# Optimization experiments

Measured on AMD Instinct MI355X. Metric: run time of the kernel, lower is better.

## Reference

```python
import jax, jax.numpy as jnp
import numpy as np


def _maxpool2(t):
    # 2x2x2 max pool, stride 2. t: [B, C, D, H, W]
    B, C, D, H, W = t.shape
    return t.reshape(B, C, D // 2, 2, H // 2, 2, W // 2, 2).max(axis=(3, 5, 7))


def setup_inputs() -> dict:
    key = jax.random.key(0)
    ks = jax.random.split(key, 5)
    ch = 64
    B, D, H, W = 2, 32, 32, 32
    x = jax.random.normal(ks[0], (B, ch, D, H, W), dtype=jnp.float32)
    # 1x1x1 conv weights (out_ch, in_ch), Kaiming-ish scale
    w_theta = jax.random.normal(ks[1], (ch // 8, ch), dtype=jnp.float32) / np.sqrt(ch)
    w_phi = jax.random.normal(ks[2], (ch // 8, ch), dtype=jnp.float32) / np.sqrt(ch)
    w_g = jax.random.normal(ks[3], (ch // 2, ch), dtype=jnp.float32) / np.sqrt(ch)
    w_o = jax.random.normal(ks[4], (ch, ch // 2), dtype=jnp.float32) / np.sqrt(ch // 2)
    gamma = jnp.ones((), dtype=jnp.float32)  # original inits at 0; 1 gives nontrivial output
    return {"x": x, "w_theta": w_theta, "w_phi": w_phi, "w_g": w_g, "w_o": w_o, "gamma": gamma}


def reference(x, w_theta, w_phi, w_g, w_o, gamma):
    B, C, D, H, W = x.shape
    N = D * H * W
    M = N // 8
    xf = x.reshape(B, C, N)  # [B, C, N]
    # 1x1x1 convs = channel matmuls
    theta = jnp.einsum('oc,bcn->bon', w_theta, xf)                     # [B, C//8, N]
    phi = _maxpool2(jnp.einsum('oc,bcn->bon', w_phi, xf).reshape(B, C // 8, D, H, W)).reshape(B, C // 8, M)
    g = _maxpool2(jnp.einsum('oc,bcn->bon', w_g, xf).reshape(B, C // 2, D, H, W)).reshape(B, C // 2, M)
    # unscaled attention: softmax over keys (M)
    beta = jax.nn.softmax(jnp.einsum('bcn,bcm->bnm', theta, phi), axis=-1)  # [B, N, M]
    o = jnp.einsum('bcm,bnm->bcn', g, beta)                                 # [B, C//2, N]
    out = gamma * jnp.einsum('oc,bcn->bon', w_o, o).reshape(B, C, D, H, W) + x
    return out
```

## Files before the change

kernel.cpp:

```cpp
#include <hip/hip_runtime.h>
#include <cstdint>
#include <cstddef>

typedef __attribute__((ext_vector_type(4))) short short4v;
typedef __attribute__((ext_vector_type(4))) float float4v;

#define C_IN  64
#define NB    2
#define NPTS  32768
#define MPTS  4096
#define LOG2E 1.44269504088896340736f
#define KT    64
#define NTILE (MPTS / KT)
#define QT64  (NPTS / 64)

__device__ __forceinline__ unsigned short f2bf_rne(float f) {
  unsigned int u = __builtin_bit_cast(unsigned int, f);
  u += 0x7fffu + ((u >> 16) & 1u);
  return (unsigned short)(u >> 16);
}

__device__ __forceinline__ short4v pack_bf16_trunc(float a0, float a1, float a2, float a3) {
  unsigned int u0 = __builtin_amdgcn_perm(__builtin_bit_cast(unsigned int, a1),
                                          __builtin_bit_cast(unsigned int, a0), 0x07060302u);
  unsigned int u1 = __builtin_amdgcn_perm(__builtin_bit_cast(unsigned int, a3),
                                          __builtin_bit_cast(unsigned int, a2), 0x07060302u);
  union { unsigned int u[2]; short4v s; } r;
  r.u[0] = u0; r.u[1] = u1;
  return r.s;
}

__device__ __forceinline__ short4v pack_bf16_rne(float a0, float a1, float a2, float a3) {
  short4v s;
  s[0] = (short)f2bf_rne(a0); s[1] = (short)f2bf_rne(a1);
  s[2] = (short)f2bf_rne(a2); s[3] = (short)f2bf_rne(a3);
  return s;
}

__device__ __forceinline__ void gl_lds16(const unsigned short* g, unsigned short* l) {
  __builtin_amdgcn_global_load_lds(
      (const __attribute__((address_space(1))) void*)g,
      (__attribute__((address_space(3))) void*)l, 16, 0, 0);
}


__device__ void pool_body(int idx, const float* __restrict__ x,
                          const float* __restrict__ w_phi,
                          const float* __restrict__ w_g,
                          unsigned short* __restrict__ phi_f,
                          unsigned short* __restrict__ g_f) {
  int cg = idx >> 13;
  int bm = idx & 8191;
  int b = bm >> 12, m = bm & 4095;
  int md = m >> 8, mh = (m >> 4) & 15, mw = m & 15;
  const float* xb = x + (size_t)b * C_IN * NPTS
                  + ((md * 2) * 1024 + (mh * 2) * 32 + (mw * 2));
  const float* wbase = (cg == 0) ? w_phi : (w_g + (cg - 1) * 8 * C_IN);

  float acc[8][8];
#pragma unroll
  for (int o = 0; o < 8; ++o)
#pragma unroll
    for (int p = 0; p < 8; ++p) acc[o][p] = 0.f;

#pragma unroll 4
  for (int cc = 0; cc < C_IN; ++cc) {
    const float* xp = xb + (size_t)cc * NPTS;
    float2 p01 = *(const float2*)(xp + 0);
    float2 p23 = *(const float2*)(xp + 32);
    float2 p45 = *(const float2*)(xp + 1024);
    float2 p67 = *(const float2*)(xp + 1056);
#pragma unroll
    for (int o = 0; o < 8; ++o) {
      float wv = wbase[o * C_IN + cc];
      acc[o][0] = fmaf(wv, p01.x, acc[o][0]);
      acc[o][1] = fmaf(wv, p01.y, acc[o][1]);
      acc[o][2] = fmaf(wv, p23.x, acc[o][2]);
      acc[o][3] = fmaf(wv, p23.y, acc[o][3]);
      acc[o][4] = fmaf(wv, p45.x, acc[o][4]);
      acc[o][5] = fmaf(wv, p45.y, acc[o][5]);
      acc[o][6] = fmaf(wv, p67.x, acc[o][6]);
      acc[o][7] = fmaf(wv, p67.y, acc[o][7]);
    }
  }
  float mx[8];
#pragma unroll
  for (int o = 0; o < 8; ++o) {
    mx[o] = fmaxf(fmaxf(fmaxf(acc[o][0], acc[o][1]), fmaxf(acc[o][2], acc[o][3])),
                  fmaxf(fmaxf(acc[o][4], acc[o][5]), fmaxf(acc[o][6], acc[o][7])));
  }
  int kt16 = m >> 4, kr = m & 15;
  if (cg == 0) {
    size_t fb = ((size_t)b * 256 + kt16) * 256;
#pragma unroll
    for (int g2 = 0; g2 < 2; ++g2) {
      unsigned int u0 = (unsigned int)f2bf_rne(mx[g2 * 4 + 0] * LOG2E)
                      | ((unsigned int)f2bf_rne(mx[g2 * 4 + 1] * LOG2E) << 16);
      unsigned int u1 = (unsigned int)f2bf_rne(mx[g2 * 4 + 2] * LOG2E)
                      | ((unsigned int)f2bf_rne(mx[g2 * 4 + 3] * LOG2E) << 16);
      *(uint2*)&phi_f[fb + (g2 * 16 + kr) * 4] = make_uint2(u0, u1);
      *(uint2*)&phi_f[fb + ((g2 + 2) * 16 + kr) * 4] = make_uint2(0u, 0u);
    }
  } else {
    int gc0 = (cg - 1) * 8;
#pragma unroll
    for (int o = 0; o < 8; ++o) {
      int c = gc0 + o;
      int half = c >> 4, c15 = c & 15;
      size_t base = (((size_t)b * 256 + kt16) * 2 + half) * 256;
      g_f[base + ((kr >> 2) * 16 + c15) * 4 + (kr & 3)] = f2bf_rne(mx[o]);
    }
  }
}

__device__ void theta_body(int idx, const float* __restrict__ x,
                           const float* __restrict__ w_theta,
                           unsigned short* __restrict__ theta_pad) {
  int b = idx >> 15, n = idx & 32767;
  const float* xb = x + (size_t)b * C_IN * NPTS + n;
  float t[8];
#pragma unroll
  for (int o = 0; o < 8; ++o) t[o] = 0.f;
#pragma unroll 4
  for (int cc = 0; cc < C_IN; ++cc) {
    float xv = xb[(size_t)cc * NPTS];
#pragma unroll
    for (int o = 0; o < 8; ++o) t[o] = fmaf(w_theta[o * C_IN + cc], xv, t[o]);
  }
  unsigned int w0 = (unsigned int)f2bf_rne(t[0]) | ((unsigned int)f2bf_rne(t[1]) << 16);
  unsigned int w1 = (unsigned int)f2bf_rne(t[2]) | ((unsigned int)f2bf_rne(t[3]) << 16);
  unsigned int w2 = (unsigned int)f2bf_rne(t[4]) | ((unsigned int)f2bf_rne(t[5]) << 16);
  unsigned int w3 = (unsigned int)f2bf_rne(t[6]) | ((unsigned int)f2bf_rne(t[7]) << 16);
  uint4* dst = (uint4*)(theta_pad + ((size_t)idx << 4));
  dst[0] = make_uint4(w0, w1, w2, w3);
  dst[1] = make_uint4(0u, 0u, 0u, 0u);
}

__global__ __launch_bounds__(256) void prep_fused(
    const float* __restrict__ x, const float* __restrict__ w_theta,
    const float* __restrict__ w_phi, const float* __restrict__ w_g,
    unsigned short* __restrict__ theta_pad,
    unsigned short* __restrict__ phi_f,
    unsigned short* __restrict__ g_f) {
  int gb = blockIdx.x;
  if (gb < 160) {
    pool_body(gb * 256 + threadIdx.x, x, w_phi, w_g, phi_f, g_f);
  } else {
    theta_body((gb - 160) * 256 + threadIdx.x, x, w_theta, theta_pad);
  }
}

template <int KS>
__global__ __launch_bounds__(256, 4) void attn_split64(
    const unsigned short* __restrict__ theta_pad,
    const unsigned short* __restrict__ phi_f,
    const unsigned short* __restrict__ g_f,
    float4v* __restrict__ opart,
    float* __restrict__ lbuf) {
  __shared__ unsigned short s_phi[2][KT * 16];
  __shared__ unsigned short s_g[2][(KT / 16) * 512];

  int tid = threadIdx.x;
  int wid = tid >> 6, lane = tid & 63;
  int l4 = lane >> 4, col = lane & 15;
  int b = blockIdx.y / KS;
  int ks = blockIdx.y % KS;
  int qb = blockIdx.x * 256 + wid * 64;
  int qt64 = blockIdx.x * 4 + wid;
  int t0 = ks * (NTILE / KS);
  int t1 = t0 + NTILE / KS;

  const unsigned short* tb = theta_pad + ((size_t)(b * NPTS + qb) << 4) + l4 * 4;
  short4v bt0 = *(const short4v*)(tb + ((0 * 16 + col) << 4));
  short4v bt1 = *(const short4v*)(tb + ((1 * 16 + col) << 4));
  short4v bt2 = *(const short4v*)(tb + ((2 * 16 + col) << 4));
  short4v bt3 = *(const short4v*)(tb + ((3 * 16 + col) << 4));

  const unsigned short* phib = phi_f + (size_t)b * 65536;
  const unsigned short* gb   = g_f + (size_t)b * 131072;

  float4v acc[2][4];
#pragma unroll
  for (int h = 0; h < 2; ++h)
#pragma unroll
    for (int j = 0; j < 4; ++j) acc[h][j] = (float4v){0.f, 0.f, 0.f, 0.f};
  float lsum0 = 0.f, lsum1 = 0.f, lsum2 = 0.f, lsum3 = 0.f;

  gl_lds16(gb + (size_t)t0 * 2048 + wid * 512 + lane * 8, &s_g[0][wid * 512]);
  if (wid < 2)
    gl_lds16(phib + (size_t)t0 * 1024 + wid * 512 + lane * 8, &s_phi[0][wid * 512]);
  __syncthreads();

#pragma unroll 1
  for (int t = t0; t < t1; ++t) {
    int cur = t & 1;
    if (t + 1 < t1) {
      gl_lds16(gb + (size_t)(t + 1) * 2048 + wid * 512 + lane * 8,
               &s_g[cur ^ 1][wid * 512]);
      if (wid < 2)
        gl_lds16(phib + (size_t)(t + 1) * 1024 + wid * 512 + lane * 8,
                 &s_phi[cur ^ 1][wid * 512]);
    }

#pragma unroll
    for (int st = 0; st < 4; ++st) {
      short4v pf = *(const short4v*)&s_phi[cur][st * 256 + lane * 4];
      short4v g0 = *(const short4v*)&s_g[cur][st * 512 + lane * 4];
      short4v g1 = *(const short4v*)&s_g[cur][st * 512 + 256 + lane * 4];

      float4v zero4 = {0.f, 0.f, 0.f, 0.f};
      float4v s0 = __builtin_amdgcn_mfma_f32_16x16x16bf16_1k(pf, bt0, zero4, 0, 0, 0);
      float4v s1 = __builtin_amdgcn_mfma_f32_16x16x16bf16_1k(pf, bt1, zero4, 0, 0, 0);
      float4v s2 = __builtin_amdgcn_mfma_f32_16x16x16bf16_1k(pf, bt2, zero4, 0, 0, 0);
      float4v s3 = __builtin_amdgcn_mfma_f32_16x16x16bf16_1k(pf, bt3, zero4, 0, 0, 0);

      float p00 = __builtin_amdgcn_exp2f(s0[0]);
      float p01 = __builtin_amdgcn_exp2f(s0[1]);
      float p02 = __builtin_amdgcn_exp2f(s0[2]);
      float p03 = __builtin_amdgcn_exp2f(s0[3]);
      float p10 = __builtin_amdgcn_exp2f(s1[0]);
      float p11 = __builtin_amdgcn_exp2f(s1[1]);
      float p12 = __builtin_amdgcn_exp2f(s1[2]);
      float p13 = __builtin_amdgcn_exp2f(s1[3]);
      float p20 = __builtin_amdgcn_exp2f(s2[0]);
      float p21 = __builtin_amdgcn_exp2f(s2[1]);
      float p22 = __builtin_amdgcn_exp2f(s2[2]);
      float p23 = __builtin_amdgcn_exp2f(s2[3]);
      float p30 = __builtin_amdgcn_exp2f(s3[0]);
      float p31 = __builtin_amdgcn_exp2f(s3[1]);
      float p32 = __builtin_amdgcn_exp2f(s3[2]);
      float p33 = __builtin_amdgcn_exp2f(s3[3]);
      lsum0 += (p00 + p01) + (p02 + p03);
      lsum1 += (p10 + p11) + (p12 + p13);
      lsum2 += (p20 + p21) + (p22 + p23);
      lsum3 += (p30 + p31) + (p32 + p33);
      short4v pb0 = pack_bf16_trunc(p00, p01, p02, p03);
      short4v pb1 = pack_bf16_trunc(p10, p11, p12, p13);
      short4v pb2 = pack_bf16_trunc(p20, p21, p22, p23);
      short4v pb3 = pack_bf16_trunc(p30, p31, p32, p33);

      acc[0][0] = __builtin_amdgcn_mfma_f32_16x16x16bf16_1k(g0, pb0, acc[0][0], 0, 0, 0);
      acc[0][1] = __builtin_amdgcn_mfma_f32_16x16x16bf16_1k(g0, pb1, acc[0][1], 0, 0, 0);
      acc[0][2] = __builtin_amdgcn_mfma_f32_16x16x16bf16_1k(g0, pb2, acc[0][2], 0, 0, 0);
      acc[0][3] = __builtin_amdgcn_mfma_f32_16x16x16bf16_1k(g0, pb3, acc[0][3], 0, 0, 0);
      acc[1][0] = __builtin_amdgcn_mfma_f32_16x16x16bf16_1k(g1, pb0, acc[1][0], 0, 0, 0);
      acc[1][1] = __builtin_amdgcn_mfma_f32_16x16x16bf16_1k(g1, pb1, acc[1][1], 0, 0, 0);
      acc[1][2] = __builtin_amdgcn_mfma_f32_16x16x16bf16_1k(g1, pb2, acc[1][2], 0, 0, 0);
      acc[1][3] = __builtin_amdgcn_mfma_f32_16x16x16bf16_1k(g1, pb3, acc[1][3], 0, 0, 0);
    }
    __syncthreads();
  }

  lsum0 += __shfl_xor(lsum0, 16, 64);
  lsum0 += __shfl_xor(lsum0, 32, 64);
  lsum1 += __shfl_xor(lsum1, 16, 64);
  lsum1 += __shfl_xor(lsum1, 32, 64);
  lsum2 += __shfl_xor(lsum2, 16, 64);
  lsum2 += __shfl_xor(lsum2, 32, 64);
  lsum3 += __shfl_xor(lsum3, 16, 64);
  lsum3 += __shfl_xor(lsum3, 32, 64);

  size_t rowb = (size_t)(b * KS + ks) * QT64 + qt64;
  float myl = (l4 == 0) ? lsum0 : (l4 == 1) ? lsum1 : (l4 == 2) ? lsum2 : lsum3;
  lbuf[rowb * 64 + lane] = myl;

  size_t obase = rowb * 8 * 64 + lane;
#pragma unroll
  for (int h = 0; h < 2; ++h)
#pragma unroll
    for (int j = 0; j < 4; ++j)
      opart[obase + (size_t)(h * 4 + j) * 64] = acc[h][j];
}

template <int KS>
__global__ __launch_bounds__(256) void attn_combine(
    const float* __restrict__ x, const float* __restrict__ w_o,
    const float* __restrict__ gamma_p,
    const float4v* __restrict__ opart,
    const float* __restrict__ lbuf,
    float* __restrict__ out) {
  int tid = threadIdx.x;
  int wid = tid >> 6, lane = tid & 63;
  int l4 = lane >> 4, col = lane & 15;
  int b = blockIdx.y;
  int qt32 = blockIdx.x * 4 + wid;
  int qb = qt32 * 32;
  int qt64 = qt32 >> 1, hf = qt32 & 1;

  float gamma = gamma_p[0];

  short4v wo[4][2];
#pragma unroll
  for (int cot = 0; cot < 4; ++cot)
#pragma unroll
    for (int ksw = 0; ksw < 2; ++ksw) {
      const float* wp = w_o + (cot * 16 + col) * 32 + ksw * 16 + l4 * 4;
      wo[cot][ksw] = pack_bf16_rne(wp[0] * gamma, wp[1] * gamma,
                                   wp[2] * gamma, wp[3] * gamma);
    }

  float4v a0 = {0.f, 0.f, 0.f, 0.f}, a1 = a0, a2 = a0, a3 = a0;
  float ls0 = 0.f, ls1 = 0.f;
#pragma unroll
  for (int ks = 0; ks < KS; ++ks) {
    size_t rowb = (size_t)(b * KS + ks) * QT64 + qt64;
    size_t ob = (rowb * 8 + hf * 2) * 64 + lane;
    a0 += opart[ob + 0 * 64];
    a1 += opart[ob + 1 * 64];
    a2 += opart[ob + 4 * 64];
    a3 += opart[ob + 5 * 64];
    const float* lb = lbuf + rowb * 64 + hf * 32;
    ls0 += lb[col];
    ls1 += lb[col + 16];
  }
  float li0 = 1.0f / ls0;
  float li1 = 1.0f / ls1;

  short4v onb00 = pack_bf16_rne(a0[0] * li0, a0[1] * li0, a0[2] * li0, a0[3] * li0);
  short4v onb01 = pack_bf16_rne(a1[0] * li1, a1[1] * li1, a1[2] * li1, a1[3] * li1);
  short4v onb10 = pack_bf16_rne(a2[0] * li0, a2[1] * li0, a2[2] * li0, a2[3] * li0);
  short4v onb11 = pack_bf16_rne(a3[0] * li1, a3[1] * li1, a3[2] * li1, a3[3] * li1);

  float4v zero4 = {0.f, 0.f, 0.f, 0.f};
#pragma unroll
  for (int cot = 0; cot < 4; ++cot) {
#pragma unroll
    for (int nt = 0; nt < 2; ++nt) {
      short4v bfrag0 = nt ? onb01 : onb00;
      short4v bfrag1 = nt ? onb11 : onb10;
      float4v d = __builtin_amdgcn_mfma_f32_16x16x16bf16_1k(wo[cot][0], bfrag0, zero4, 0, 0, 0);
      d = __builtin_amdgcn_mfma_f32_16x16x16bf16_1k(wo[cot][1], bfrag1, d, 0, 0, 0);
      int n = qb + nt * 16 + col;
      size_t base = (size_t)(b * C_IN + cot * 16 + l4 * 4) * NPTS + n;
      const float* xp = x + base;
      float* op = out + base;
#pragma unroll
      for (int e = 0; e < 4; ++e) {
        op[(size_t)e * NPTS] = d[e] + xp[(size_t)e * NPTS];
      }
    }
  }
}

__global__ __launch_bounds__(256) void attn_mfma(
    const float* __restrict__ x, const float* __restrict__ w_o,
    const float* __restrict__ gamma_p,
    const unsigned short* __restrict__ theta_pad,
    const unsigned short* __restrict__ phi_f,
    const unsigned short* __restrict__ g_f,
    float* __restrict__ out) {
  __shared__ unsigned short s_phi[2][KT * 16];
  __shared__ unsigned short s_g[2][(KT / 16) * 512];

  int tid = threadIdx.x;
  int wid = tid >> 6, lane = tid & 63;
  int l4 = lane >> 4, col = lane & 15;
  int b = blockIdx.y;
  int qb = blockIdx.x * 128 + wid * 32;

  float gamma = gamma_p[0];

  const unsigned short* tb = theta_pad + ((size_t)(b * NPTS + qb) << 4) + l4 * 4;
  short4v bt0 = *(const short4v*)(tb + (col << 4));
  short4v bt1 = *(const short4v*)(tb + ((16 + col) << 4));

  short4v wo[4][2];
#pragma unroll
  for (int cot = 0; cot < 4; ++cot)
#pragma unroll
    for (int ksw = 0; ksw < 2; ++ksw) {
      const float* wp = w_o + (cot * 16 + col) * 32 + ksw * 16 + l4 * 4;
      wo[cot][ksw] = pack_bf16_rne(wp[0] * gamma, wp[1] * gamma,
                                   wp[2] * gamma, wp[3] * gamma);
    }

  const unsigned short* phib = phi_f + (size_t)b * 256 * 256;
  const unsigned short* gb   = g_f + (size_t)b * 256 * 512;

  float4v acc00 = {0.f, 0.f, 0.f, 0.f}, acc01 = acc00, acc10 = acc00, acc11 = acc00;
  float lsum0 = 0.f, lsum1 = 0.f;

  gl_lds16(gb + 0 * 2048 + wid * 512 + lane * 8, &s_g[0][wid * 512]);
  if (wid < 2)
    gl_lds16(phib + 0 * 1024 + wid * 512 + lane * 8, &s_phi[0][wid * 512]);
  __syncthreads();

#pragma unroll 1
  for (int t = 0; t < NTILE; ++t) {
    int cur = t & 1;
    if (t + 1 < NTILE) {
      gl_lds16(gb + (size_t)(t + 1) * 2048 + wid * 512 + lane * 8,
               &s_g[cur ^ 1][wid * 512]);
      if (wid < 2)
        gl_lds16(phib + (size_t)(t + 1) * 1024 + wid * 512 + lane * 8,
                 &s_phi[cur ^ 1][wid * 512]);
    }
#pragma unroll
    for (int st = 0; st < 4; ++st) {
      short4v pf = *(const short4v*)&s_phi[cur][st * 256 + lane * 4];
      short4v g0 = *(const short4v*)&s_g[cur][st * 512 + lane * 4];
      short4v g1 = *(const short4v*)&s_g[cur][st * 512 + 256 + lane * 4];

      float4v zero4 = {0.f, 0.f, 0.f, 0.f};
      float4v s0 = __builtin_amdgcn_mfma_f32_16x16x16bf16_1k(pf, bt0, zero4, 0, 0, 0);
      float4v s1 = __builtin_amdgcn_mfma_f32_16x16x16bf16_1k(pf, bt1, zero4, 0, 0, 0);

      float p00 = __builtin_amdgcn_exp2f(s0[0]);
      float p01 = __builtin_amdgcn_exp2f(s0[1]);
      float p02 = __builtin_amdgcn_exp2f(s0[2]);
      float p03 = __builtin_amdgcn_exp2f(s0[3]);
      float p10 = __builtin_amdgcn_exp2f(s1[0]);
      float p11 = __builtin_amdgcn_exp2f(s1[1]);
      float p12 = __builtin_amdgcn_exp2f(s1[2]);
      float p13 = __builtin_amdgcn_exp2f(s1[3]);
      lsum0 += (p00 + p01) + (p02 + p03);
      lsum1 += (p10 + p11) + (p12 + p13);
      short4v pb0 = pack_bf16_trunc(p00, p01, p02, p03);
      short4v pb1 = pack_bf16_trunc(p10, p11, p12, p13);

      acc00 = __builtin_amdgcn_mfma_f32_16x16x16bf16_1k(g0, pb0, acc00, 0, 0, 0);
      acc01 = __builtin_amdgcn_mfma_f32_16x16x16bf16_1k(g0, pb1, acc01, 0, 0, 0);
      acc10 = __builtin_amdgcn_mfma_f32_16x16x16bf16_1k(g1, pb0, acc10, 0, 0, 0);
      acc11 = __builtin_amdgcn_mfma_f32_16x16x16bf16_1k(g1, pb1, acc11, 0, 0, 0);
    }
    __syncthreads();
  }

  lsum0 += __shfl_xor(lsum0, 16, 64);
  lsum0 += __shfl_xor(lsum0, 32, 64);
  lsum1 += __shfl_xor(lsum1, 16, 64);
  lsum1 += __shfl_xor(lsum1, 32, 64);
  float li0 = 1.0f / lsum0;
  float li1 = 1.0f / lsum1;

  short4v onb00 = pack_bf16_rne(acc00[0] * li0, acc00[1] * li0, acc00[2] * li0, acc00[3] * li0);
  short4v onb01 = pack_bf16_rne(acc01[0] * li1, acc01[1] * li1, acc01[2] * li1, acc01[3] * li1);
  short4v onb10 = pack_bf16_rne(acc10[0] * li0, acc10[1] * li0, acc10[2] * li0, acc10[3] * li0);
  short4v onb11 = pack_bf16_rne(acc11[0] * li1, acc11[1] * li1, acc11[2] * li1, acc11[3] * li1);

  float4v zero4 = {0.f, 0.f, 0.f, 0.f};
#pragma unroll
  for (int cot = 0; cot < 4; ++cot) {
#pragma unroll
    for (int nt = 0; nt < 2; ++nt) {
      short4v bfrag0 = nt ? onb01 : onb00;
      short4v bfrag1 = nt ? onb11 : onb10;
      float4v d = __builtin_amdgcn_mfma_f32_16x16x16bf16_1k(wo[cot][0], bfrag0, zero4, 0, 0, 0);
      d = __builtin_amdgcn_mfma_f32_16x16x16bf16_1k(wo[cot][1], bfrag1, d, 0, 0, 0);
      int n = qb + nt * 16 + col;
      size_t base = (size_t)(b * C_IN + cot * 16 + l4 * 4) * NPTS + n;
      const float* xp = x + base;
      float* op = out + base;
#pragma unroll
      for (int e = 0; e < 4; ++e) {
        op[(size_t)e * NPTS] = d[e] + xp[(size_t)e * NPTS];
      }
    }
  }
}

extern "C" void kernel_launch(void* const* d_in, const int* in_sizes, int n_in,
                              void* d_out, int out_size, void* d_ws, size_t ws_size,
                              hipStream_t stream) {
  const float* x       = (const float*)d_in[0];
  const float* w_theta = (const float*)d_in[1];
  const float* w_phi   = (const float*)d_in[2];
  const float* w_g     = (const float*)d_in[3];
  const float* w_o     = (const float*)d_in[4];
  const float* gamma   = (const float*)d_in[5];
  float* out = (float*)d_out;

  char* ws = (char*)d_ws;
  unsigned short* phi_f     = (unsigned short*)ws;  ws += (size_t)NB * 256 * 256 * 2;
  unsigned short* g_f       = (unsigned short*)ws;  ws += (size_t)NB * 256 * 512 * 2;
  unsigned short* theta_pad = (unsigned short*)ws;  ws += (size_t)NB * NPTS * 16 * 2;
  size_t base_need = (size_t)(ws - (char*)d_ws);
  float4v* opart = (float4v*)ws;
  size_t opart4 = (size_t)NB * 4 * QT64 * 8 * 64 * sizeof(float4v);
  size_t opart2 = (size_t)NB * 2 * QT64 * 8 * 64 * sizeof(float4v);
  size_t lbuf4  = (size_t)NB * 4 * QT64 * 64 * sizeof(float);
  size_t lbuf2  = (size_t)NB * 2 * QT64 * 64 * sizeof(float);
  size_t need4 = base_need + opart4 + lbuf4;
  size_t need2 = base_need + opart2 + lbuf2;

  prep_fused<<<dim3(416), dim3(256), 0, stream>>>(
      x, w_theta, w_phi, w_g, theta_pad, phi_f, g_f);

  if (ws_size >= need4) {
    float* lbuf = (float*)((char*)opart + opart4);
    attn_split64<4><<<dim3(NPTS / 256, NB * 4), dim3(256), 0, stream>>>(
        theta_pad, phi_f, g_f, opart, lbuf);
    attn_combine<4><<<dim3(NPTS / 128, NB), dim3(256), 0, stream>>>(
        x, w_o, gamma, opart, lbuf, out);
  } else if (ws_size >= need2) {
    float* lbuf = (float*)((char*)opart + opart2);
    attn_split64<2><<<dim3(NPTS / 256, NB * 2), dim3(256), 0, stream>>>(
        theta_pad, phi_f, g_f, opart, lbuf);
    attn_combine<2><<<dim3(NPTS / 128, NB), dim3(256), 0, stream>>>(
        x, w_o, gamma, opart, lbuf, out);
  } else if (ws_size >= base_need) {
    attn_mfma<<<dim3(NPTS / 128, NB), dim3(256), 0, stream>>>(
        x, w_o, gamma, theta_pad, phi_f, g_f, out);
  }
}
```

Baseline: 92.91 us.

## Double key tile per stage, store split partials as bf16, raise occupancy hint

The split-K attention kernel now stages 128 keys per double-buffered tile instead of 64, with every wave loading its share of phi and g. This halves the number of loop iterations and barriers. The per-split partial outputs are packed to bf16 before they are written, which halves the opart traffic that the combine kernel reads and unpacks. The launch bound asks for 8 blocks per CU, which may force register spilling, and LDS use per block doubles. Rounding the partials to bf16 before they are summed adds accuracy loss.

```diff
diff --git a/kernel.cpp b/kernel.cpp
--- a/kernel.cpp
+++ b/kernel.cpp
@@ -10,8 +10,10 @@
 #define NPTS  32768
 #define MPTS  4096
 #define LOG2E 1.44269504088896340736f
-#define KT    64
-#define NTILE (MPTS / KT)
+#define KT    128
+#define NT128 (MPTS / KT)
+#define KTF   64
+#define NTILE (MPTS / KTF)
 #define QT64  (NPTS / 64)
 
 __device__ __forceinline__ unsigned short f2bf_rne(float f) {
@@ -35,6 +37,20 @@
   s[0] = (short)f2bf_rne(a0); s[1] = (short)f2bf_rne(a1);
   s[2] = (short)f2bf_rne(a2); s[3] = (short)f2bf_rne(a3);
   return s;
+}
+
+__device__ __forceinline__ uint2 pack_bf16x4_u2(float4v a) {
+  uint2 r;
+  r.x = (unsigned int)f2bf_rne(a[0]) | ((unsigned int)f2bf_rne(a[1]) << 16);
+  r.y = (unsigned int)f2bf_rne(a[2]) | ((unsigned int)f2bf_rne(a[3]) << 16);
+  return r;
+}
+
+__device__ __forceinline__ void unpack_bf16x4_add(uint2 u, float4v* a) {
+  (*a)[0] += __builtin_bit_cast(float, u.x << 16);
+  (*a)[1] += __builtin_bit_cast(float, u.x & 0xffff0000u);
+  (*a)[2] += __builtin_bit_cast(float, u.y << 16);
+  (*a)[3] += __builtin_bit_cast(float, u.y & 0xffff0000u);
 }
 
 __device__ __forceinline__ void gl_lds16(const unsigned short* g, unsigned short* l) {
@@ -151,11 +167,11 @@
 }
 
 template <int KS>
-__global__ __launch_bounds__(256, 4) void attn_split64(
+__global__ __launch_bounds__(256, 8) void attn_split64(
     const unsigned short* __restrict__ theta_pad,
     const unsigned short* __restrict__ phi_f,
     const unsigned short* __restrict__ g_f,
-    float4v* __restrict__ opart,
+    uint2* __restrict__ opart,
     float* __restrict__ lbuf) {
   __shared__ unsigned short s_phi[2][KT * 16];
   __shared__ unsigned short s_g[2][(KT / 16) * 512];
@@ -167,8 +183,8 @@
   int ks = blockIdx.y % KS;
   int qb = blockIdx.x * 256 + wid * 64;
   int qt64 = blockIdx.x * 4 + wid;
-  int t0 = ks * (NTILE / KS);
-  int t1 = t0 + NTILE / KS;
+  int t0 = ks * (NT128 / KS);
+  int t1 = t0 + NT128 / KS;
 
   const unsigned short* tb = theta_pad + ((size_t)(b * NPTS + qb) << 4) + l4 * 4;
   short4v bt0 = *(const short4v*)(tb + ((0 * 16 + col) << 4));
@@ -186,24 +202,25 @@
     for (int j = 0; j < 4; ++j) acc[h][j] = (float4v){0.f, 0.f, 0.f, 0.f};
   float lsum0 = 0.f, lsum1 = 0.f, lsum2 = 0.f, lsum3 = 0.f;
 
-  gl_lds16(gb + (size_t)t0 * 2048 + wid * 512 + lane * 8, &s_g[0][wid * 512]);
-  if (wid < 2)
-    gl_lds16(phib + (size_t)t0 * 1024 + wid * 512 + lane * 8, &s_phi[0][wid * 512]);
+  gl_lds16(gb + (size_t)t0 * 4096 + (size_t)wid * 512 + lane * 8, &s_g[0][wid * 512]);
+  gl_lds16(gb + (size_t)t0 * 4096 + (size_t)(wid + 4) * 512 + lane * 8, &s_g[0][(wid + 4) * 512]);
+  gl_lds16(phib + (size_t)t0 * 2048 + (size_t)wid * 512 + lane * 8, &s_phi[0][wid * 512]);
   __syncthreads();
 
 #pragma unroll 1
   for (int t = t0; t < t1; ++t) {
     int cur = t & 1;
     if (t + 1 < t1) {
-      gl_lds16(gb + (size_t)(t + 1) * 2048 + wid * 512 + lane * 8,
+      gl_lds16(gb + (size_t)(t + 1) * 4096 + (size_t)wid * 512 + lane * 8,
                &s_g[cur ^ 1][wid * 512]);
-      if (wid < 2)
-        gl_lds16(phib + (size_t)(t + 1) * 1024 + wid * 512 + lane * 8,
-                 &s_phi[cur ^ 1][wid * 512]);
-    }
-
-#pragma unroll
-    for (int st = 0; st < 4; ++st) {
+      gl_lds16(gb + (size_t)(t + 1) * 4096 + (size_t)(wid + 4) * 512 + lane * 8,
+               &s_g[cur ^ 1][(wid + 4) * 512]);
+      gl_lds16(phib + (size_t)(t + 1) * 2048 + (size_t)wid * 512 + lane * 8,
+               &s_phi[cur ^ 1][wid * 512]);
+    }
+
+#pragma unroll
+    for (int st = 0; st < 8; ++st) {
       short4v pf = *(const short4v*)&s_phi[cur][st * 256 + lane * 4];
       short4v g0 = *(const short4v*)&s_g[cur][st * 512 + lane * 4];
       short4v g1 = *(const short4v*)&s_g[cur][st * 512 + 256 + lane * 4];
@@ -269,14 +286,14 @@
   for (int h = 0; h < 2; ++h)
 #pragma unroll
     for (int j = 0; j < 4; ++j)
-      opart[obase + (size_t)(h * 4 + j) * 64] = acc[h][j];
+      opart[obase + (size_t)(h * 4 + j) * 64] = pack_bf16x4_u2(acc[h][j]);
 }
 
 template <int KS>
 __global__ __launch_bounds__(256) void attn_combine(
     const float* __restrict__ x, const float* __restrict__ w_o,
     const float* __restrict__ gamma_p,
-    const float4v* __restrict__ opart,
+    const uint2* __restrict__ opart,
     const float* __restrict__ lbuf,
     float* __restrict__ out) {
   int tid = threadIdx.x;
@@ -305,10 +322,10 @@
   for (int ks = 0; ks < KS; ++ks) {
     size_t rowb = (size_t)(b * KS + ks) * QT64 + qt64;
     size_t ob = (rowb * 8 + hf * 2) * 64 + lane;
-    a0 += opart[ob + 0 * 64];
-    a1 += opart[ob + 1 * 64];
-    a2 += opart[ob + 4 * 64];
-    a3 += opart[ob + 5 * 64];
+    unpack_bf16x4_add(opart[ob + 0 * 64], &a0);
+    unpack_bf16x4_add(opart[ob + 1 * 64], &a1);
+    unpack_bf16x4_add(opart[ob + 4 * 64], &a2);
+    unpack_bf16x4_add(opart[ob + 5 * 64], &a3);
     const float* lb = lbuf + rowb * 64 + hf * 32;
     ls0 += lb[col];
     ls1 += lb[col + 16];
@@ -349,8 +366,8 @@
     const unsigned short* __restrict__ phi_f,
     const unsigned short* __restrict__ g_f,
     float* __restrict__ out) {
-  __shared__ unsigned short s_phi[2][KT * 16];
-  __shared__ unsigned short s_g[2][(KT / 16) * 512];
+  __shared__ unsigned short s_phi[2][KTF * 16];
+  __shared__ unsigned short s_g[2][(KTF / 16) * 512];
 
   int tid = threadIdx.x;
   int wid = tid >> 6, lane = tid & 63;
@@ -475,9 +492,9 @@
   unsigned short* g_f       = (unsigned short*)ws;  ws += (size_t)NB * 256 * 512 * 2;
   unsigned short* theta_pad = (unsigned short*)ws;  ws += (size_t)NB * NPTS * 16 * 2;
   size_t base_need = (size_t)(ws - (char*)d_ws);
-  float4v* opart = (float4v*)ws;
-  size_t opart4 = (size_t)NB * 4 * QT64 * 8 * 64 * sizeof(float4v);
-  size_t opart2 = (size_t)NB * 2 * QT64 * 8 * 64 * sizeof(float4v);
+  uint2* opart = (uint2*)ws;
+  size_t opart4 = (size_t)NB * 4 * QT64 * 8 * 64 * sizeof(uint2);
+  size_t opart2 = (size_t)NB * 2 * QT64 * 8 * 64 * sizeof(uint2);
   size_t lbuf4  = (size_t)NB * 4 * QT64 * 64 * sizeof(float);
   size_t lbuf2  = (size_t)NB * 2 * QT64 * 64 * sizeof(float);
   size_t need4 = base_need + opart4 + lbuf4;
```

Measured after the change: 96.26 us. 3.6% more time.

## Store split-K attention partials as bf16 and halve pool work per thread

Applied to the files above, without the earlier changes.

The split-K attention kernel now writes its unnormalized partial outputs as packed bf16 (uint2) instead of float4, and the combine kernel unpacks them and accumulates in fp32. This halves the traffic of the intermediate partial buffer. Separately, the pooled phi/g projection now gives each thread 4 output channels instead of 8, doubling the pool blocks from 160 to 320 (grid 576) to expose more parallelism in the prep kernel, at the cost of re-reading x more times. The bf16 partials add rounding error before the softmax normalization.

```diff
diff --git a/kernel.cpp b/kernel.cpp
--- a/kernel.cpp
+++ b/kernel.cpp
@@ -35,6 +35,20 @@
   s[0] = (short)f2bf_rne(a0); s[1] = (short)f2bf_rne(a1);
   s[2] = (short)f2bf_rne(a2); s[3] = (short)f2bf_rne(a3);
   return s;
+}
+
+__device__ __forceinline__ uint2 pack_bf16x4_u2(float4v a) {
+  uint2 r;
+  r.x = (unsigned int)f2bf_rne(a[0]) | ((unsigned int)f2bf_rne(a[1]) << 16);
+  r.y = (unsigned int)f2bf_rne(a[2]) | ((unsigned int)f2bf_rne(a[3]) << 16);
+  return r;
+}
+
+__device__ __forceinline__ void unpack_bf16x4_add(uint2 u, float4v* a) {
+  (*a)[0] += __builtin_bit_cast(float, u.x << 16);
+  (*a)[1] += __builtin_bit_cast(float, u.x & 0xffff0000u);
+  (*a)[2] += __builtin_bit_cast(float, u.y << 16);
+  (*a)[3] += __builtin_bit_cast(float, u.y & 0xffff0000u);
 }
 
 __device__ __forceinline__ void gl_lds16(const unsigned short* g, unsigned short* l) {
@@ -55,11 +69,12 @@
   int md = m >> 8, mh = (m >> 4) & 15, mw = m & 15;
   const float* xb = x + (size_t)b * C_IN * NPTS
                   + ((md * 2) * 1024 + (mh * 2) * 32 + (mw * 2));
-  const float* wbase = (cg == 0) ? w_phi : (w_g + (cg - 1) * 8 * C_IN);
-
-  float acc[8][8];
-#pragma unroll
-  for (int o = 0; o < 8; ++o)
+  const float* wbase = (cg < 2) ? (w_phi + cg * 4 * C_IN)
+                                : (w_g + (cg - 2) * 4 * C_IN);
+
+  float acc[4][8];
+#pragma unroll
+  for (int o = 0; o < 4; ++o)
 #pragma unroll
     for (int p = 0; p < 8; ++p) acc[o][p] = 0.f;
 
@@ -71,7 +86,7 @@
     float2 p45 = *(const float2*)(xp + 1024);
     float2 p67 = *(const float2*)(xp + 1056);
 #pragma unroll
-    for (int o = 0; o < 8; ++o) {
+    for (int o = 0; o < 4; ++o) {
       float wv = wbase[o * C_IN + cc];
       acc[o][0] = fmaf(wv, p01.x, acc[o][0]);
       acc[o][1] = fmaf(wv, p01.y, acc[o][1]);
@@ -83,28 +98,25 @@
       acc[o][7] = fmaf(wv, p67.y, acc[o][7]);
     }
   }
-  float mx[8];
-#pragma unroll
-  for (int o = 0; o < 8; ++o) {
+  float mx[4];
+#pragma unroll
+  for (int o = 0; o < 4; ++o) {
     mx[o] = fmaxf(fmaxf(fmaxf(acc[o][0], acc[o][1]), fmaxf(acc[o][2], acc[o][3])),
                   fmaxf(fmaxf(acc[o][4], acc[o][5]), fmaxf(acc[o][6], acc[o][7])));
   }
   int kt16 = m >> 4, kr = m & 15;
-  if (cg == 0) {
+  if (cg < 2) {
     size_t fb = ((size_t)b * 256 + kt16) * 256;
-#pragma unroll
-    for (int g2 = 0; g2 < 2; ++g2) {
-      unsigned int u0 = (unsigned int)f2bf_rne(mx[g2 * 4 + 0] * LOG2E)
-                      | ((unsigned int)f2bf_rne(mx[g2 * 4 + 1] * LOG2E) << 16);
-      unsigned int u1 = (unsigned int)f2bf_rne(mx[g2 * 4 + 2] * LOG2E)
-                      | ((unsigned int)f2bf_rne(mx[g2 * 4 + 3] * LOG2E) << 16);
-      *(uint2*)&phi_f[fb + (g2 * 16 + kr) * 4] = make_uint2(u0, u1);
-      *(uint2*)&phi_f[fb + ((g2 + 2) * 16 + kr) * 4] = make_uint2(0u, 0u);
-    }
+    unsigned int u0 = (unsigned int)f2bf_rne(mx[0] * LOG2E)
+                    | ((unsigned int)f2bf_rne(mx[1] * LOG2E) << 16);
+    unsigned int u1 = (unsigned int)f2bf_rne(mx[2] * LOG2E)
+                    | ((unsigned int)f2bf_rne(mx[3] * LOG2E) << 16);
+    *(uint2*)&phi_f[fb + (cg * 16 + kr) * 4] = make_uint2(u0, u1);
+    *(uint2*)&phi_f[fb + ((cg + 2) * 16 + kr) * 4] = make_uint2(0u, 0u);
   } else {
-    int gc0 = (cg - 1) * 8;
-#pragma unroll
-    for (int o = 0; o < 8; ++o) {
+    int gc0 = (cg - 2) * 4;
+#pragma unroll
+    for (int o = 0; o < 4; ++o) {
       int c = gc0 + o;
       int half = c >> 4, c15 = c & 15;
       size_t base = (((size_t)b * 256 + kt16) * 2 + half) * 256;
@@ -143,10 +155,10 @@
     unsigned short* __restrict__ phi_f,
     unsigned short* __restrict__ g_f) {
   int gb = blockIdx.x;
-  if (gb < 160) {
+  if (gb < 320) {
     pool_body(gb * 256 + threadIdx.x, x, w_phi, w_g, phi_f, g_f);
   } else {
-    theta_body((gb - 160) * 256 + threadIdx.x, x, w_theta, theta_pad);
+    theta_body((gb - 320) * 256 + threadIdx.x, x, w_theta, theta_pad);
   }
 }
 
@@ -155,7 +167,7 @@
     const unsigned short* __restrict__ theta_pad,
     const unsigned short* __restrict__ phi_f,
     const unsigned short* __restrict__ g_f,
-    float4v* __restrict__ opart,
+    uint2* __restrict__ opart,
     float* __restrict__ lbuf) {
   __shared__ unsigned short s_phi[2][KT * 16];
   __shared__ unsigned short s_g[2][(KT / 16) * 512];
@@ -269,14 +281,14 @@
   for (int h = 0; h < 2; ++h)
 #pragma unroll
     for (int j = 0; j < 4; ++j)
-      opart[obase + (size_t)(h * 4 + j) * 64] = acc[h][j];
+      opart[obase + (size_t)(h * 4 + j) * 64] = pack_bf16x4_u2(acc[h][j]);
 }
 
 template <int KS>
 __global__ __launch_bounds__(256) void attn_combine(
     const float* __restrict__ x, const float* __restrict__ w_o,
     const float* __restrict__ gamma_p,
-    const float4v* __restrict__ opart,
+    const uint2* __restrict__ opart,
     const float* __restrict__ lbuf,
     float* __restrict__ out) {
   int tid = threadIdx.x;
@@ -305,10 +317,10 @@
   for (int ks = 0; ks < KS; ++ks) {
     size_t rowb = (size_t)(b * KS + ks) * QT64 + qt64;
     size_t ob = (rowb * 8 + hf * 2) * 64 + lane;
-    a0 += opart[ob + 0 * 64];
-    a1 += opart[ob + 1 * 64];
-    a2 += opart[ob + 4 * 64];
-    a3 += opart[ob + 5 * 64];
+    unpack_bf16x4_add(opart[ob + 0 * 64], &a0);
+    unpack_bf16x4_add(opart[ob + 1 * 64], &a1);
+    unpack_bf16x4_add(opart[ob + 4 * 64], &a2);
+    unpack_bf16x4_add(opart[ob + 5 * 64], &a3);
     const float* lb = lbuf + rowb * 64 + hf * 32;
     ls0 += lb[col];
     ls1 += lb[col + 16];
@@ -475,15 +487,15 @@
   unsigned short* g_f       = (unsigned short*)ws;  ws += (size_t)NB * 256 * 512 * 2;
   unsigned short* theta_pad = (unsigned short*)ws;  ws += (size_t)NB * NPTS * 16 * 2;
   size_t base_need = (size_t)(ws - (char*)d_ws);
-  float4v* opart = (float4v*)ws;
-  size_t opart4 = (size_t)NB * 4 * QT64 * 8 * 64 * sizeof(float4v);
-  size_t opart2 = (size_t)NB * 2 * QT64 * 8 * 64 * sizeof(float4v);
+  uint2* opart = (uint2*)ws;
+  size_t opart4 = (size_t)NB * 4 * QT64 * 8 * 64 * sizeof(uint2);
+  size_t opart2 = (size_t)NB * 2 * QT64 * 8 * 64 * sizeof(uint2);
   size_t lbuf4  = (size_t)NB * 4 * QT64 * 64 * sizeof(float);
   size_t lbuf2  = (size_t)NB * 2 * QT64 * 64 * sizeof(float);
   size_t need4 = base_need + opart4 + lbuf4;
   size_t need2 = base_need + opart2 + lbuf2;
 
-  prep_fused<<<dim3(416), dim3(256), 0, stream>>>(
+  prep_fused<<<dim3(576), dim3(256), 0, stream>>>(
       x, w_theta, w_phi, w_g, theta_pad, phi_f, g_f);
 
   if (ws_size >= need4) {
```

After: 80.83 us. -13.0%, faster.
